# Performance work log

Measured on AMD Instinct MI355X. Metric: run time of the kernel, lower is better.

## Reference

```python
import jax, jax.numpy as jnp
import numpy as np

D_MODEL = 1024
NHEAD = 16
HEAD_DIM = D_MODEL // NHEAD


def setup_inputs() -> dict:
    key = jax.random.key(0)
    ks = jax.random.split(key, 7)
    B, S = 4, 2048
    scale = 1.0 / np.sqrt(D_MODEL)
    x = jax.random.normal(ks[0], (B, S, D_MODEL), dtype=jnp.float32)
    Wq = jax.random.normal(ks[1], (D_MODEL, D_MODEL), dtype=jnp.float32) * scale
    Wk = jax.random.normal(ks[2], (D_MODEL, D_MODEL), dtype=jnp.float32) * scale
    Wv = jax.random.normal(ks[3], (D_MODEL, D_MODEL), dtype=jnp.float32) * scale
    bq = jax.random.normal(ks[4], (D_MODEL,), dtype=jnp.float32) * 0.01
    bk = jax.random.normal(ks[5], (D_MODEL,), dtype=jnp.float32) * 0.01
    bv = jax.random.normal(ks[6], (D_MODEL,), dtype=jnp.float32) * 0.01
    return {"x": x, "Wq": Wq, "bq": bq, "Wk": Wk, "bk": bk, "Wv": Wv, "bv": bv}


def reference(x, Wq, bq, Wk, bk, Wv, bv):
    B, S, _ = x.shape
    # Linear projections (torch Linear: x @ W.T + b; weights here are already [in, out])
    q = x @ Wq + bq
    k = x @ Wk + bk
    v = x @ Wv + bv
    # [B, S, H, Dh] -> [B, H, S, Dh]
    q = q.reshape(B, S, NHEAD, HEAD_DIM).transpose(0, 2, 1, 3)
    k = k.reshape(B, S, NHEAD, HEAD_DIM).transpose(0, 2, 1, 3)
    v = v.reshape(B, S, NHEAD, HEAD_DIM).transpose(0, 2, 1, 3)
    # NOTE: original scales by sqrt(d_model), not sqrt(head_dim)
    scores = jnp.einsum("bhqd,bhkd->bhqk", q, k) / np.sqrt(D_MODEL).astype(np.float32)
    attn = jax.nn.softmax(scores, axis=-1)  # dropout is identity at eval
    out = jnp.einsum("bhqk,bhkd->bhqd", attn, v)
    out = out.transpose(0, 2, 1, 3).reshape(B, S, D_MODEL)
    return out
```

## Files before the change

### kernel.cpp

```cpp
#include <hip/hip_runtime.h>
#include <cstdint>
#include <cstddef>

#define SEQ 2048
#define BATCH 4
#define KVB 64
#define NT (SEQ / KVB)

typedef __attribute__((ext_vector_type(8))) unsigned short u16x8;
typedef __attribute__((ext_vector_type(8))) __bf16 bf16x8;
typedef __attribute__((ext_vector_type(4))) float f32x4;
typedef __attribute__((ext_vector_type(4))) unsigned short u16x4;

#if defined(__has_builtin)
#if __has_builtin(__builtin_amdgcn_exp2f)
#define EXP2(x) __builtin_amdgcn_exp2f(x)
#else
#define EXP2(x) exp2f(x)
#endif
#else
#define EXP2(x) exp2f(x)
#endif

static __device__ __forceinline__ unsigned short f2bf(float f) {
  unsigned u = __builtin_bit_cast(unsigned, f);
  u += 0x7fffu + ((u >> 16) & 1u);
  return (unsigned short)(u >> 16);
}

static __device__ __forceinline__ f32x4 mfma16(u16x8 a, u16x8 b, f32x4 c) {
  return __builtin_amdgcn_mfma_f32_16x16x32_bf16(
      __builtin_bit_cast(bf16x8, a), __builtin_bit_cast(bf16x8, b), c, 0, 0, 0);
}

static __device__ __forceinline__ f32x4 mfma16b(u16x8 a, bf16x8 b, f32x4 c) {
  return __builtin_amdgcn_mfma_f32_16x16x32_bf16(
      __builtin_bit_cast(bf16x8, a), b, c, 0, 0, 0);
}

static __device__ __forceinline__ void gl_lds16(const void* g, void* l) {
  __builtin_amdgcn_global_load_lds(
      (const __attribute__((address_space(1))) void*)g,
      (__attribute__((address_space(3))) void*)l, 16, 0, 0);
}

__global__ __launch_bounds__(256) void k_conv_x(const float* __restrict__ x,
                                                unsigned short* __restrict__ xb) {
  int i = (blockIdx.x * 256 + threadIdx.x) * 8;
  f32x4 a = *reinterpret_cast<const f32x4*>(x + i);
  f32x4 b = *reinterpret_cast<const f32x4*>(x + i + 4);
  u16x8 v;
  v[0] = f2bf(a[0]); v[1] = f2bf(a[1]); v[2] = f2bf(a[2]); v[3] = f2bf(a[3]);
  v[4] = f2bf(b[0]); v[5] = f2bf(b[1]); v[6] = f2bf(b[2]); v[7] = f2bf(b[3]);
  *reinterpret_cast<u16x8*>(xb + i) = v;
}

__global__ __launch_bounds__(256) void k_conv_w(const float* __restrict__ Wq,
                                                const float* __restrict__ Wk,
                                                const float* __restrict__ Wv,
                                                unsigned short* __restrict__ wt) {
  const float* W = (blockIdx.z == 0) ? Wq : (blockIdx.z == 1) ? Wk : Wv;
  unsigned short* dst = wt + (size_t)blockIdx.z * 1024 * 1024;
  __shared__ float tile[32][33];
  int n0 = blockIdx.x * 32, k0 = blockIdx.y * 32;
  int tx = threadIdx.x, ty = threadIdx.y;
#pragma unroll
  for (int i = 0; i < 4; i++) {
    int k = ty + i * 8;
    tile[k][tx] = W[(size_t)(k0 + k) * 1024 + n0 + tx];
  }
  __syncthreads();
#pragma unroll
  for (int i = 0; i < 4; i++) {
    int n = ty + i * 8;
    dst[(size_t)(n0 + n) * 1024 + k0 + tx] = f2bf(tile[tx][n]);
  }
}

__global__ __launch_bounds__(256) void k_qkv_gemm(
    const unsigned short* __restrict__ xb, const unsigned short* __restrict__ wt,
    const float* __restrict__ bq, const float* __restrict__ bk,
    const float* __restrict__ bv,
    unsigned short* __restrict__ qb, unsigned short* __restrict__ kb,
    unsigned short* __restrict__ vt) {
  __shared__ unsigned short Ah[3][128 * 32];
  __shared__ unsigned short Bh[3][128 * 32];
  const int tid = threadIdx.x;
  const int lane = tid & 63, wid = tid >> 6;
  const int ln = lane & 15, g = lane >> 4;
  const int wr = wid >> 1, wc = wid & 1;
  const int dd = blockIdx.x;
  const int xcd = dd & 7, j = dd >> 3;
  const int z = j >> 6, kk = j & 63;
  const int m0 = (((kk >> 3) << 3) | xcd) * 128;
  const int n0 = (kk & 7) * 128;
  const unsigned short* Bt = wt + (size_t)z * 1024 * 1024;

  f32x4 acc[4][4];
#pragma unroll
  for (int i = 0; i < 4; i++)
#pragma unroll
    for (int jj = 0; jj < 4; jj++) acc[i][jj] = f32x4{0.f, 0.f, 0.f, 0.f};

  const int rA0 = tid >> 2, cA0 = tid & 3;
  const int swA = (cA0 ^ ((rA0 >> 1) & 3)) << 3;
  const int rA1 = rA0 + 64;

  const unsigned short* gA0 = xb + (size_t)(m0 + rA0) * 1024 + swA;
  const unsigned short* gA1 = xb + (size_t)(m0 + rA1) * 1024 + swA;
  const unsigned short* gB0 = Bt + (size_t)(n0 + rA0) * 1024 + swA;
  const unsigned short* gB1 = Bt + (size_t)(n0 + rA1) * 1024 + swA;

#define GSTAGE(bb, k0)                                          \
  do {                                                          \
    gl_lds16(gA0 + (k0), &Ah[bb][wid * 512]);                   \
    gl_lds16(gA1 + (k0), &Ah[bb][2048 + wid * 512]);            \
    gl_lds16(gB0 + (k0), &Bh[bb][wid * 512]);                   \
    gl_lds16(gB1 + (k0), &Bh[bb][2048 + wid * 512]);            \
  } while (0)

  const int fsw = (g ^ ((ln >> 1) & 3)) << 3;

#define GCOMPUTE(bb)                                                       \
  do {                                                                     \
    u16x8 af[4], bfv[4];                                                   \
    _Pragma("unroll") for (int mi = 0; mi < 4; mi++)                       \
      af[mi] = *reinterpret_cast<const u16x8*>(                            \
          &Ah[bb][(wr * 64 + mi * 16 + ln) * 32 + fsw]);                   \
    _Pragma("unroll") for (int ni = 0; ni < 4; ni++)                       \
      bfv[ni] = *reinterpret_cast<const u16x8*>(                           \
          &Bh[bb][(wc * 64 + ni * 16 + ln) * 32 + fsw]);                   \
    __builtin_amdgcn_s_setprio(1);                                         \
    _Pragma("unroll") for (int mi = 0; mi < 4; mi++)                       \
    _Pragma("unroll") for (int ni = 0; ni < 4; ni++)                       \
      acc[mi][ni] = mfma16(af[mi], bfv[ni], acc[mi][ni]);                  \
    __builtin_amdgcn_s_setprio(0);                                         \
  } while (0)

  GSTAGE(0, 0);
  GSTAGE(1, 32);
  asm volatile("s_waitcnt vmcnt(4)" ::: "memory");
  __builtin_amdgcn_s_barrier();

  for (int t = 0; t < 30; t++) {
    GCOMPUTE(t % 3);
    GSTAGE((t + 2) % 3, (t + 2) * 32);
    asm volatile("s_waitcnt vmcnt(4)" ::: "memory");
    __builtin_amdgcn_s_barrier();
  }
  GCOMPUTE(0);
  asm volatile("s_waitcnt vmcnt(0)" ::: "memory");
  __builtin_amdgcn_s_barrier();
  GCOMPUTE(1);

  const float* bias = (z == 0) ? bq : (z == 1) ? bk : bv;
#pragma unroll
  for (int ni = 0; ni < 4; ni++) {
    int n = n0 + wc * 64 + ni * 16 + ln;
    float bb = bias[n];
    int h = n >> 6, d = n & 63;
#pragma unroll
    for (int mi = 0; mi < 4; mi++) {
      int mb = m0 + wr * 64 + mi * 16 + 4 * g;
      int b = mb >> 11, s = mb & 2047;
      if (z == 2) {
        u16x4 pv;
#pragma unroll
        for (int i = 0; i < 4; i++) pv[i] = f2bf(acc[mi][ni][i] + bb);
        int s4 = s >> 2;
        int u = s4 & 7, blk = s4 >> 3;
        int nu = ((u & 3) << 1) | (u >> 2);
        int sp = ((blk << 3) | nu) << 2;
        *reinterpret_cast<u16x4*>(
            &vt[((size_t)((b * 16 + h) * 64 + d)) * 2048 + sp]) = pv;
      } else {
        unsigned short* dst = (z == 0) ? qb : kb;
        float sc = (z == 0) ? 0.0450842200f : 1.0f;
#pragma unroll
        for (int i = 0; i < 4; i++) {
          dst[((size_t)((b * 16 + h) * 2048) + (s + i)) * 64 + d] =
              f2bf((acc[mi][ni][i] + bb) * sc);
        }
      }
    }
  }
#undef GSTAGE
#undef GCOMPUTE
}

__global__ __launch_bounds__(512) void k_attn(
    const unsigned short* __restrict__ qb, const unsigned short* __restrict__ kb,
    const unsigned short* __restrict__ vt, float* __restrict__ out) {
  __shared__ unsigned short Kl[3][KVB * 64];
  __shared__ unsigned short Vl[3][64 * KVB];
  const int tid = threadIdx.x;
  const int lane = tid & 63, wid = tid >> 6;
  const int ln = lane & 15, g = lane >> 4;
  const int flat = blockIdx.x;
  const int bh = flat & 63, qidx = flat >> 6;
  const int b = bh >> 4, h = bh & 15;
  const int q0 = qidx * 256 + wid * 32;
  const unsigned short* Qp = qb + (size_t)bh * SEQ * 64;
  const unsigned short* Kp = kb + (size_t)bh * SEQ * 64;
  const unsigned short* Vp = vt + (size_t)bh * 64 * SEQ;

  const int kr0 = tid >> 3;
  const int psw = ((tid & 7) ^ (kr0 & 7)) << 3;
  const unsigned short* srcK0 = Kp + (size_t)kr0 * 64 + psw;
  const unsigned short* srcV0 = Vp + (size_t)kr0 * SEQ + psw;

#define STAGE(bb, tt)                                                     \
  do {                                                                    \
    gl_lds16(srcK0 + (size_t)(tt) * (KVB * 64), &Kl[bb][wid * 512]);      \
    gl_lds16(srcV0 + (size_t)(tt) * KVB, &Vl[bb][wid * 512]);             \
  } while (0)

  u16x8 qf[2][2];
#pragma unroll
  for (int qt = 0; qt < 2; qt++)
#pragma unroll
    for (int dc = 0; dc < 2; dc++)
      qf[qt][dc] = *reinterpret_cast<const u16x8*>(
          &Qp[(size_t)(q0 + qt * 16 + ln) * 64 + dc * 32 + g * 8]);

  f32x4 o[4][2];
#pragma unroll
  for (int dt = 0; dt < 4; dt++)
#pragma unroll
    for (int qt = 0; qt < 2; qt++) o[dt][qt] = f32x4{0.f, 0.f, 0.f, 0.f};
  f32x4 lsum[2] = {f32x4{0.f, 0.f, 0.f, 0.f}, f32x4{0.f, 0.f, 0.f, 0.f}};

  u16x8 ones;
#pragma unroll
  for (int i = 0; i < 8; i++) ones[i] = 0x3F80;

  const int lm = ln & 7;
  const int ksw0 = (g ^ lm) << 3;
  const int ksw1 = ((4 + g) ^ lm) << 3;
  const int vsw0 = (g ^ lm) << 3;
  const int vsw1 = ((4 + g) ^ lm) << 3;

#define ACOMPUTE(bi)                                                          \
  do {                                                                        \
    const unsigned short* Kb = Kl[bi];                                        \
    const unsigned short* Vb = Vl[bi];                                        \
    u16x8 kf[4][2];                                                           \
    _Pragma("unroll") for (int kt = 0; kt < 4; kt++) {                        \
      int rb = (kt * 16 + ln) * 64;                                           \
      kf[kt][0] = *reinterpret_cast<const u16x8*>(&Kb[rb + ksw0]);            \
      kf[kt][1] = *reinterpret_cast<const u16x8*>(&Kb[rb + ksw1]);            \
    }                                                                         \
    f32x4 st[2][4];                                                           \
    __builtin_amdgcn_s_setprio(1);                                            \
    _Pragma("unroll") for (int qt = 0; qt < 2; qt++)                          \
    _Pragma("unroll") for (int kt = 0; kt < 4; kt++) {                        \
      f32x4 c = f32x4{0.f, 0.f, 0.f, 0.f};                                    \
      c = mfma16(kf[kt][0], qf[qt][0], c);                                    \
      c = mfma16(kf[kt][1], qf[qt][1], c);                                    \
      st[qt][kt] = c;                                                         \
    }                                                                         \
    __builtin_amdgcn_s_setprio(0);                                            \
    _Pragma("unroll") for (int qt = 0; qt < 2; qt++)                          \
    _Pragma("unroll") for (int kt = 0; kt < 4; kt++)                          \
    _Pragma("unroll") for (int i = 0; i < 4; i++)                             \
      st[qt][kt][i] = EXP2(st[qt][kt][i]);                                    \
    bf16x8 pb[2][2];                                                          \
    _Pragma("unroll") for (int qt = 0; qt < 2; qt++)                          \
    _Pragma("unroll") for (int ks = 0; ks < 2; ks++)                          \
    _Pragma("unroll") for (int i = 0; i < 4; i++) {                           \
      pb[qt][ks][i] = (__bf16)st[qt][2 * ks][i];                              \
      pb[qt][ks][4 + i] = (__bf16)st[qt][2 * ks + 1][i];                      \
    }                                                                         \
    __builtin_amdgcn_s_setprio(1);                                            \
    _Pragma("unroll") for (int dt = 0; dt < 4; dt++) {                        \
      int rb = (dt * 16 + ln) * 64;                                           \
      u16x8 vf0 = *reinterpret_cast<const u16x8*>(&Vb[rb + vsw0]);            \
      o[dt][0] = mfma16b(vf0, pb[0][0], o[dt][0]);                            \
      o[dt][1] = mfma16b(vf0, pb[1][0], o[dt][1]);                            \
      u16x8 vf1 = *reinterpret_cast<const u16x8*>(&Vb[rb + vsw1]);            \
      o[dt][0] = mfma16b(vf1, pb[0][1], o[dt][0]);                            \
      o[dt][1] = mfma16b(vf1, pb[1][1], o[dt][1]);                            \
    }                                                                         \
    _Pragma("unroll") for (int ks = 0; ks < 2; ks++) {                        \
      lsum[0] = mfma16b(ones, pb[0][ks], lsum[0]);                            \
      lsum[1] = mfma16b(ones, pb[1][ks], lsum[1]);                            \
    }                                                                         \
    __builtin_amdgcn_s_setprio(0);                                            \
  } while (0)

  STAGE(0, 0);
  STAGE(1, 1);
  asm volatile("s_waitcnt vmcnt(2)" ::: "memory");
  __builtin_amdgcn_s_barrier();

  for (int t = 0; t < NT - 2; t++) {
    STAGE((t + 2) % 3, t + 2);
    ACOMPUTE(t % 3);
    asm volatile("s_waitcnt vmcnt(2)" ::: "memory");
    __builtin_amdgcn_s_barrier();
  }
  ACOMPUTE((NT - 2) % 3);
  asm volatile("s_waitcnt vmcnt(0)" ::: "memory");
  __builtin_amdgcn_s_barrier();
  ACOMPUTE((NT - 1) % 3);

  float inv[2] = {1.f / lsum[0][0], 1.f / lsum[1][0]};

#pragma unroll
  for (int qt = 0; qt < 2; qt++) {
    int q = q0 + qt * 16 + ln;
#pragma unroll
    for (int dt = 0; dt < 4; dt++) {
      f32x4 r;
#pragma unroll
      for (int i = 0; i < 4; i++) r[i] = o[dt][qt][i] * inv[qt];
      *reinterpret_cast<f32x4*>(
          &out[((size_t)(b * SEQ + q)) * 1024 + h * 64 + dt * 16 + 4 * g]) = r;
    }
  }
#undef STAGE
#undef ACOMPUTE
}

extern "C" void kernel_launch(void* const* d_in, const int* in_sizes, int n_in,
                              void* d_out, int out_size, void* d_ws, size_t ws_size,
                              hipStream_t stream) {
  (void)in_sizes; (void)n_in; (void)out_size;
  const float* x  = (const float*)d_in[0];
  const float* Wq = (const float*)d_in[1];
  const float* bq = (const float*)d_in[2];
  const float* Wk = (const float*)d_in[3];
  const float* bk = (const float*)d_in[4];
  const float* Wv = (const float*)d_in[5];
  const float* bv = (const float*)d_in[6];
  float* out = (float*)d_out;

  char* ws = (char*)d_ws;
  if (ws_size < 73400320u) return;
  unsigned short* xb    = (unsigned short*)(ws);
  unsigned short* wt    = (unsigned short*)(ws + 16777216);
  unsigned short* qbuf  = (unsigned short*)(ws + 23068672);
  unsigned short* kbuf  = (unsigned short*)(ws + 39845888);
  unsigned short* vtbuf = (unsigned short*)(ws + 56623104);

  k_conv_x<<<4096, 256, 0, stream>>>(x, xb);
  k_conv_w<<<dim3(32, 32, 3), dim3(32, 8), 0, stream>>>(Wq, Wk, Wv, wt);
  k_qkv_gemm<<<dim3(1536), 256, 0, stream>>>(xb, wt, bq, bk, bv,
                                             qbuf, kbuf, vtbuf);
  k_attn<<<dim3(512), dim3(512), 0, stream>>>(qbuf, kbuf, vtbuf, out);
}
```

Before: 150.7 us.

## Enlarge QKV GEMM block tile to 256x128 with per-wave 64x128 subtiles

```diff
diff --git a/kernel.cpp b/kernel.cpp
--- a/kernel.cpp
+++ b/kernel.cpp
@@ -83,69 +83,67 @@
     const float* __restrict__ bv,
     unsigned short* __restrict__ qb, unsigned short* __restrict__ kb,
     unsigned short* __restrict__ vt) {
-  __shared__ unsigned short Ah[3][128 * 32];
+  __shared__ unsigned short Ah[3][256 * 32];
   __shared__ unsigned short Bh[3][128 * 32];
   const int tid = threadIdx.x;
   const int lane = tid & 63, wid = tid >> 6;
   const int ln = lane & 15, g = lane >> 4;
-  const int wr = wid >> 1, wc = wid & 1;
   const int dd = blockIdx.x;
   const int xcd = dd & 7, j = dd >> 3;
-  const int z = j >> 6, kk = j & 63;
-  const int m0 = (((kk >> 3) << 3) | xcd) * 128;
+  const int z = j >> 5, kk = j & 31;
+  const int m0 = ((kk >> 3) * 8 + xcd) * 256;
   const int n0 = (kk & 7) * 128;
   const unsigned short* Bt = wt + (size_t)z * 1024 * 1024;
 
-  f32x4 acc[4][4];
+  f32x4 acc[4][8];
 #pragma unroll
   for (int i = 0; i < 4; i++)
 #pragma unroll
-    for (int jj = 0; jj < 4; jj++) acc[i][jj] = f32x4{0.f, 0.f, 0.f, 0.f};
+    for (int jj = 0; jj < 8; jj++) acc[i][jj] = f32x4{0.f, 0.f, 0.f, 0.f};
 
   const int rA0 = tid >> 2, cA0 = tid & 3;
   const int swA = (cA0 ^ ((rA0 >> 1) & 3)) << 3;
-  const int rA1 = rA0 + 64;
 
   const unsigned short* gA0 = xb + (size_t)(m0 + rA0) * 1024 + swA;
-  const unsigned short* gA1 = xb + (size_t)(m0 + rA1) * 1024 + swA;
   const unsigned short* gB0 = Bt + (size_t)(n0 + rA0) * 1024 + swA;
-  const unsigned short* gB1 = Bt + (size_t)(n0 + rA1) * 1024 + swA;
-
-#define GSTAGE(bb, k0)                                          \
-  do {                                                          \
-    gl_lds16(gA0 + (k0), &Ah[bb][wid * 512]);                   \
-    gl_lds16(gA1 + (k0), &Ah[bb][2048 + wid * 512]);            \
-    gl_lds16(gB0 + (k0), &Bh[bb][wid * 512]);                   \
-    gl_lds16(gB1 + (k0), &Bh[bb][2048 + wid * 512]);            \
+
+#define GSTAGE(bb, k0)                                                \
+  do {                                                                \
+    gl_lds16(gA0 + (k0), &Ah[bb][wid * 512]);                         \
+    gl_lds16(gA0 + 64 * 1024 + (k0), &Ah[bb][2048 + wid * 512]);      \
+    gl_lds16(gA0 + 128 * 1024 + (k0), &Ah[bb][4096 + wid * 512]);     \
+    gl_lds16(gA0 + 192 * 1024 + (k0), &Ah[bb][6144 + wid * 512]);     \
+    gl_lds16(gB0 + (k0), &Bh[bb][wid * 512]);                         \
+    gl_lds16(gB0 + 64 * 1024 + (k0), &Bh[bb][2048 + wid * 512]);      \
   } while (0)
 
   const int fsw = (g ^ ((ln >> 1) & 3)) << 3;
 
 #define GCOMPUTE(bb)                                                       \
   do {                                                                     \
-    u16x8 af[4], bfv[4];                                                   \
+    u16x8 af[4];                                                           \
     _Pragma("unroll") for (int mi = 0; mi < 4; mi++)                       \
       af[mi] = *reinterpret_cast<const u16x8*>(                            \
-          &Ah[bb][(wr * 64 + mi * 16 + ln) * 32 + fsw]);                   \
-    _Pragma("unroll") for (int ni = 0; ni < 4; ni++)                       \
-      bfv[ni] = *reinterpret_cast<const u16x8*>(                           \
-          &Bh[bb][(wc * 64 + ni * 16 + ln) * 32 + fsw]);                   \
+          &Ah[bb][(wid * 64 + mi * 16 + ln) * 32 + fsw]);                  \
     __builtin_amdgcn_s_setprio(1);                                         \
-    _Pragma("unroll") for (int mi = 0; mi < 4; mi++)                       \
-    _Pragma("unroll") for (int ni = 0; ni < 4; ni++)                       \
-      acc[mi][ni] = mfma16(af[mi], bfv[ni], acc[mi][ni]);                  \
+    _Pragma("unroll") for (int ni = 0; ni < 8; ni++) {                     \
+      u16x8 bv = *reinterpret_cast<const u16x8*>(                          \
+          &Bh[bb][(ni * 16 + ln) * 32 + fsw]);                             \
+      _Pragma("unroll") for (int mi = 0; mi < 4; mi++)                     \
+        acc[mi][ni] = mfma16(af[mi], bv, acc[mi][ni]);                     \
+    }                                                                      \
     __builtin_amdgcn_s_setprio(0);                                         \
   } while (0)
 
   GSTAGE(0, 0);
   GSTAGE(1, 32);
-  asm volatile("s_waitcnt vmcnt(4)" ::: "memory");
+  asm volatile("s_waitcnt vmcnt(6)" ::: "memory");
   __builtin_amdgcn_s_barrier();
 
   for (int t = 0; t < 30; t++) {
     GCOMPUTE(t % 3);
     GSTAGE((t + 2) % 3, (t + 2) * 32);
-    asm volatile("s_waitcnt vmcnt(4)" ::: "memory");
+    asm volatile("s_waitcnt vmcnt(6)" ::: "memory");
     __builtin_amdgcn_s_barrier();
   }
   GCOMPUTE(0);
@@ -155,13 +153,13 @@
 
   const float* bias = (z == 0) ? bq : (z == 1) ? bk : bv;
 #pragma unroll
-  for (int ni = 0; ni < 4; ni++) {
-    int n = n0 + wc * 64 + ni * 16 + ln;
+  for (int ni = 0; ni < 8; ni++) {
+    int n = n0 + ni * 16 + ln;
     float bb = bias[n];
     int h = n >> 6, d = n & 63;
 #pragma unroll
     for (int mi = 0; mi < 4; mi++) {
-      int mb = m0 + wr * 64 + mi * 16 + 4 * g;
+      int mb = m0 + wid * 64 + mi * 16 + 4 * g;
       int b = mb >> 11, s = mb & 2047;
       if (z == 2) {
         u16x4 pv;
@@ -345,7 +343,7 @@
 
   k_conv_x<<<4096, 256, 0, stream>>>(x, xb);
   k_conv_w<<<dim3(32, 32, 3), dim3(32, 8), 0, stream>>>(Wq, Wk, Wv, wt);
-  k_qkv_gemm<<<dim3(1536), 256, 0, stream>>>(xb, wt, bq, bk, bv,
-                                             qbuf, kbuf, vtbuf);
+  k_qkv_gemm<<<dim3(768), 256, 0, stream>>>(xb, wt, bq, bk, bv,
+                                            qbuf, kbuf, vtbuf);
   k_attn<<<dim3(512), dim3(512), 0, stream>>>(qbuf, kbuf, vtbuf, out);
 }
```

After: 177.0 us. 17.5% more time.
